# Kernel tuning notes

Measured on AMD Instinct MI355X. Metric: run time of the kernel, lower is better.

## Reference

```python
import jax, jax.numpy as jnp
import numpy as np

K = 20
EPS = 1e-5  # BatchNorm eps
SLOPE = 0.2  # LeakyReLU negative slope


def _lrelu(y):
    return jnp.where(y > 0, y, SLOPE * y)


def _knn_idx(x):
    # x: [B, C, N] -> idx [B, N, K] of nearest neighbors (largest of negative sq dist)
    inner = -2.0 * jnp.einsum('bcn,bcm->bnm', x, x)
    xx = jnp.sum(x * x, axis=1)  # [B, N]
    pd = -xx[:, :, None] - inner - xx[:, None, :]  # [B, N, N]
    return jax.lax.top_k(pd, K)[1]


def _graph_feature(x):
    # x: [B, C, N] -> [B, 2C, N, K] = cat(neighbor - center, center)
    idx = _knn_idx(x)
    xt = jnp.transpose(x, (0, 2, 1))  # [B, N, C]
    nb = jax.vmap(lambda f, i: f[i])(xt, idx)  # [B, N, K, C]
    ctr = xt[:, :, None, :]
    feat = jnp.concatenate([nb - ctr, jnp.broadcast_to(ctr, nb.shape)], axis=-1)
    return jnp.transpose(feat, (0, 3, 1, 2))


def _bn(y, p, ch_axis):
    g, b, m, v = p[0], p[1], p[2], p[3]
    shape = [1] * y.ndim
    shape[ch_axis] = -1
    scale = (g / jnp.sqrt(v + EPS)).reshape(shape)
    return (y - m.reshape(shape)) * scale + b.reshape(shape)


def _conv_block(x, w, bn):
    f = _graph_feature(x)  # [B, 2C_in, N, K]
    y = jnp.einsum('bcnk,oc->bonk', f, w)  # 1x1 conv, no bias
    y = _lrelu(_bn(y, bn, 1))
    return jnp.max(y, axis=-1)  # max over K neighbors -> [B, C_out, N]


def setup_inputs() -> dict:
    key = jax.random.key(0)
    ks = jax.random.split(key, 20)
    B, N = 8, 1024
    inp = {
        'x': jax.random.normal(ks[0], (B, 3, N), jnp.float32),
        'w0': jax.random.normal(ks[1], (64, 6), jnp.float32) * 0.1,
        'w1': jax.random.normal(ks[2], (64, 128), jnp.float32) * 0.1,
        'w2': jax.random.normal(ks[3], (128, 128), jnp.float32) * 0.1,
        'w3': jax.random.normal(ks[4], (256, 256), jnp.float32) * 0.1,
        'bn0': jax.random.uniform(ks[5], (4, 64), jnp.float32) + 0.1,
        'bn1': jax.random.uniform(ks[6], (4, 64), jnp.float32) + 0.1,
        'bn2': jax.random.uniform(ks[7], (4, 128), jnp.float32) + 0.1,
        'bn3': jax.random.uniform(ks[8], (4, 256), jnp.float32) + 0.1,
        'we': jax.random.normal(ks[9], (1024, 512), jnp.float32) * 0.05,
        'bne': jax.random.uniform(ks[10], (4, 1024), jnp.float32) + 0.1,
        'wf0': jax.random.normal(ks[11], (512, 2048), jnp.float32) * 0.02,
        'bnf0': jax.random.uniform(ks[12], (4, 512), jnp.float32) + 0.1,
        'wf1': jax.random.normal(ks[13], (256, 512), jnp.float32) * 0.05,
        'bnf1': jax.random.uniform(ks[14], (4, 256), jnp.float32) + 0.1,
        'wfin': jax.random.normal(ks[15], (64, 256), jnp.float32) * 0.05,
        'bfin': jax.random.normal(ks[16], (64,), jnp.float32) * 0.05,
    }
    return inp


def reference(x, w0, w1, w2, w3, bn0, bn1, bn2, bn3, we, bne, wf0, bnf0, wf1, bnf1, wfin, bfin):
    B = x.shape[0]
    x1 = _conv_block(x, w0, bn0)   # [B, 64, N]
    x2 = _conv_block(x1, w1, bn1)  # [B, 64, N]
    x3 = _conv_block(x2, w2, bn2)  # [B, 128, N]
    x4 = _conv_block(x3, w3, bn3)  # [B, 256, N]
    cat = jnp.concatenate([x1, x2, x3, x4], axis=1)  # [B, 512, N]
    e = _lrelu(_bn(jnp.einsum('bcn,oc->bon', cat, we), bne, 1))  # [B, 1024, N]
    p1 = jnp.max(e, axis=-1)
    p2 = jnp.mean(e, axis=-1)
    h = jnp.concatenate([p1, p2], axis=1)  # [B, 2048]
    h = _lrelu(_bn(h @ wf0.T, bnf0, 1))  # [B, 512]; dropout is eval-mode identity
    h = _lrelu(_bn(h @ wf1.T, bnf1, 1))  # [B, 256]
    return h @ wfin.T + bfin  # [B, 64]
```

## Files before the change

### kernel.cpp

```cpp
#include <hip/hip_runtime.h>
#include <math.h>

#define N_PTS 1024
#define BATCH 8
#define KNN 20
#define EPSB 1e-5f
#define SLOPE 0.2f

typedef __attribute__((ext_vector_type(8))) short short8;
typedef __attribute__((ext_vector_type(4))) float f32x4;
typedef unsigned short ushort_t;
typedef unsigned long long u64;

__device__ __forceinline__ float lrelu(float y) { return y > 0.f ? y : SLOPE * y; }

__device__ __forceinline__ ushort_t f2bf(float f) {
    union { float f; unsigned u; } v; v.f = f;
    unsigned r = v.u + 0x7FFF + ((v.u >> 16) & 1);
    return (ushort_t)(r >> 16);
}

__device__ __forceinline__ void wprep_one(const float* __restrict__ w, float* __restrict__ wpt,
                                          int C, int Cout, int g) {
    int M2 = 2 * Cout;
    if (g >= C * M2) return;
    int c = g / M2, m = g - c * M2;
    float v;
    if (m < Cout) v = w[(size_t)m * 2 * C + c];
    else { int o = m - Cout; v = w[(size_t)o * 2 * C + C + c] - w[(size_t)o * 2 * C + c]; }
    wpt[(size_t)c * M2 + m] = v;
}

__global__ void prep_kernel(const float* __restrict__ we, ushort_t* __restrict__ weh,
                            const float* __restrict__ w0, float* __restrict__ wpt0,
                            const float* __restrict__ w1, float* __restrict__ wpt1,
                            const float* __restrict__ w2, float* __restrict__ wpt2,
                            const float* __restrict__ w3, float* __restrict__ wpt3) {
    int bx = blockIdx.x, tid = threadIdx.x;
    if (bx < 512) {
        int g = bx * 256 + tid;
        float4 v = ((const float4*)we)[g];
        ushort4 o;
        o.x = f2bf(v.x); o.y = f2bf(v.y); o.z = f2bf(v.z); o.w = f2bf(v.w);
        ((ushort4*)weh)[g] = o;
    } else if (bx < 514) {
        wprep_one(w0, wpt0, 3, 64, (bx - 512) * 256 + tid);
    } else if (bx < 546) {
        wprep_one(w1, wpt1, 64, 64, (bx - 514) * 256 + tid);
    } else if (bx < 610) {
        wprep_one(w2, wpt2, 64, 128, (bx - 546) * 256 + tid);
    } else {
        wprep_one(w3, wpt3, 128, 256, (bx - 610) * 256 + tid);
    }
}

__global__ void __launch_bounds__(256)
pdabv_kernel(const float* __restrict__ x, const float* __restrict__ wpt,
             float* __restrict__ pd, float* __restrict__ A, float* __restrict__ Bv,
             int C, int Cout, int bstride) {
    int b = blockIdx.z;
    int nt = blockIdx.y;
    int bx = blockIdx.x;
    int tid = threadIdx.x;
    int tx = tid & 15, ty = tid >> 4;
    int n0 = nt * 128;
    __shared__ float sU0[16][128];
    __shared__ float sU1[16][128];
    __shared__ float sXX[256];
    const float* xb = x + (size_t)b * bstride;
    float acc[8][8] = {};
    if (bx < 8) {
        int m0 = bx * 128;
        float xxa = 0.f;
        for (int c0 = 0; c0 < C; c0 += 16) {
            for (int q = 0; q < 2; q++) {
                int f = q * 256 + tid;
                int r = f >> 5, col = (f & 31) * 4;
                int c = c0 + r;
                float4 vn = {0.f, 0.f, 0.f, 0.f}, vm = {0.f, 0.f, 0.f, 0.f};
                if (c < C) {
                    vn = *(const float4*)&xb[(size_t)c * N_PTS + n0 + col];
                    vm = *(const float4*)&xb[(size_t)c * N_PTS + m0 + col];
                }
                *(float4*)&sU0[r][col] = vn;
                *(float4*)&sU1[r][col] = vm;
            }
            __syncthreads();
            if (tid < 128) {
                for (int k = 0; k < 16; k++) { float v = sU0[k][tid]; xxa += v * v; }
            } else {
                int u = tid - 128;
                for (int k = 0; k < 16; k++) { float v = sU1[k][u]; xxa += v * v; }
            }
            for (int k = 0; k < 16; k++) {
                float4 a0 = *(const float4*)&sU0[k][ty * 4];
                float4 a1 = *(const float4*)&sU0[k][64 + ty * 4];
                float4 b0 = *(const float4*)&sU1[k][tx * 4];
                float4 b1 = *(const float4*)&sU1[k][64 + tx * 4];
                float av[8] = {a0.x, a0.y, a0.z, a0.w, a1.x, a1.y, a1.z, a1.w};
                float bw[8] = {b0.x, b0.y, b0.z, b0.w, b1.x, b1.y, b1.z, b1.w};
                for (int i = 0; i < 8; i++)
                    for (int j = 0; j < 8; j++) acc[i][j] += av[i] * bw[j];
            }
            __syncthreads();
        }
        sXX[tid] = xxa;
        __syncthreads();
        float xnv[8], xmv[8];
        for (int i = 0; i < 8; i++) xnv[i] = sXX[(i >> 2) * 64 + ty * 4 + (i & 3)];
        for (int j = 0; j < 8; j++) xmv[j] = sXX[128 + (j >> 2) * 64 + tx * 4 + (j & 3)];
        for (int i = 0; i < 8; i++) {
            int n = n0 + (i >> 2) * 64 + ty * 4 + (i & 3);
            float* prow = pd + ((size_t)(b * N_PTS + n)) * N_PTS;
            for (int jh = 0; jh < 2; jh++) {
                float4 o;
                o.x = 2.f * acc[i][jh * 4 + 0] - xnv[i] - xmv[jh * 4 + 0];
                o.y = 2.f * acc[i][jh * 4 + 1] - xnv[i] - xmv[jh * 4 + 1];
                o.z = 2.f * acc[i][jh * 4 + 2] - xnv[i] - xmv[jh * 4 + 2];
                o.w = 2.f * acc[i][jh * 4 + 3] - xnv[i] - xmv[jh * 4 + 3];
                *(float4*)&prow[m0 + jh * 64 + tx * 4] = o;
            }
        }
    } else {
        int m0 = (bx - 8) * 128;
        int M2 = 2 * Cout;
        for (int c0 = 0; c0 < C; c0 += 16) {
            for (int q = 0; q < 2; q++) {
                int f = q * 256 + tid;
                int r = f >> 5, col = (f & 31) * 4;
                int c = c0 + r;
                float4 vw = {0.f, 0.f, 0.f, 0.f}, vx = {0.f, 0.f, 0.f, 0.f};
                if (c < C) {
                    vw = *(const float4*)&wpt[(size_t)c * M2 + m0 + col];
                    vx = *(const float4*)&xb[(size_t)c * N_PTS + n0 + col];
                }
                *(float4*)&sU0[r][col] = vw;
                *(float4*)&sU1[r][col] = vx;
            }
            __syncthreads();
            for (int k = 0; k < 16; k++) {
                float4 a0 = *(const float4*)&sU0[k][ty * 4];
                float4 a1 = *(const float4*)&sU0[k][64 + ty * 4];
                float4 b0 = *(const float4*)&sU1[k][tx * 4];
                float4 b1 = *(const float4*)&sU1[k][64 + tx * 4];
                float av[8] = {a0.x, a0.y, a0.z, a0.w, a1.x, a1.y, a1.z, a1.w};
                float bw[8] = {b0.x, b0.y, b0.z, b0.w, b1.x, b1.y, b1.z, b1.w};
                for (int i = 0; i < 8; i++)
                    for (int j = 0; j < 8; j++) acc[i][j] += av[i] * bw[j];
            }
            __syncthreads();
        }
        for (int i = 0; i < 8; i++) {
            int rowm = m0 + (i >> 2) * 64 + ty * 4 + (i & 3);
            float* dst = (rowm < Cout) ? (A + ((size_t)b * Cout + rowm) * N_PTS)
                                       : (Bv + ((size_t)b * Cout + rowm - Cout) * N_PTS);
            for (int jh = 0; jh < 2; jh++) {
                float4 o;
                o.x = acc[i][jh * 4 + 0];
                o.y = acc[i][jh * 4 + 1];
                o.z = acc[i][jh * 4 + 2];
                o.w = acc[i][jh * 4 + 3];
                *(float4*)&dst[n0 + jh * 64 + tx * 4] = o;
            }
        }
    }
}

__global__ void __launch_bounds__(256)
topk_kernel(const float* __restrict__ pd, int* __restrict__ idx) {
    int wid = threadIdx.x >> 6;
    int row = blockIdx.x * 4 + wid;
    int lane = threadIdx.x & 63;
    __shared__ u64 Sk[4][64];
    const float* p = pd + (size_t)row * N_PTS;
    float v[16];
    for (int q = 0; q < 4; q++) {
        float4 t = *(const float4*)&p[lane * 16 + q * 4];
        v[q * 4 + 0] = t.x; v[q * 4 + 1] = t.y; v[q * 4 + 2] = t.z; v[q * 4 + 3] = t.w;
    }
    float lmax = v[0];
    #pragma unroll
    for (int j = 1; j < 16; j++) lmax = fmaxf(lmax, v[j]);
    float s = lmax;
    #pragma unroll
    for (int k = 2; k <= 64; k <<= 1) {
        #pragma unroll
        for (int j = k >> 1; j > 0; j >>= 1) {
            float o = __shfl_xor(s, j, 64);
            bool takeMin = (((lane & k) == 0) == ((lane & j) == 0));
            float mn = fminf(s, o), mx = fmaxf(s, o);
            s = takeMin ? mn : mx;
        }
    }
    float tp = __shfl(s, 44, 64);
    unsigned hm = 0;
    #pragma unroll
    for (int j = 0; j < 16; j++) hm |= (v[j] >= tp ? 1u : 0u) << j;
    int cnt = __popc(hm);
    int incl = cnt;
    #pragma unroll
    for (int d = 1; d < 64; d <<= 1) {
        int o = __shfl_up(incl, d, 64);
        if (lane >= d) incl += o;
    }
    int total = __shfl(incl, 63, 64);
    int pos = incl - cnt;
    if (total <= 64) {
        #pragma unroll
        for (int j = 0; j < 16; j++) {
            if (hm & (1u << j)) {
                unsigned u = __float_as_uint(v[j]);
                unsigned msk = ((unsigned)((int)u >> 31)) | 0x80000000u;
                Sk[wid][pos] = ((u64)(u ^ msk) << 32) | (unsigned)(1023 - (lane * 16 + j));
                pos++;
            }
        }
        u64 key = (lane < total) ? Sk[wid][lane] : 0ull;
        #pragma unroll
        for (int k = 2; k <= 64; k <<= 1) {
            #pragma unroll
            for (int j = k >> 1; j > 0; j >>= 1) {
                u64 o = __shfl_xor(key, j, 64);
                bool takeMin = (((lane & k) == 0) == ((lane & j) == 0));
                bool sgt = key > o;
                key = (sgt != takeMin) ? key : o;
            }
        }
        if (lane >= 44) {
            int m = 1023 - (int)(unsigned)(key & 0xFFFFFFFFu);
            idx[row * KNN + (63 - lane)] = m;
        }
    } else {
        for (int kk = 0; kk < KNN; kk++) {
            float bv = v[0]; int bj = 0;
            #pragma unroll
            for (int j = 1; j < 16; j++) if (v[j] > bv) { bv = v[j]; bj = j; }
            int bi = lane * 16 + bj;
            for (int d = 32; d > 0; d >>= 1) {
                float ov = __shfl_down(bv, d, 64);
                int oi = __shfl_down(bi, d, 64);
                if (ov > bv || (ov == bv && oi < bi)) { bv = ov; bi = oi; }
            }
            bi = __shfl(bi, 0, 64);
            if ((bi >> 4) == lane) {
                #pragma unroll
                for (int j = 0; j < 16; j++) if (j == (bi & 15)) v[j] = -INFINITY;
            }
            if (lane == 0) idx[row * KNN + kk] = bi;
        }
    }
}

__global__ void __launch_bounds__(256)
gmax_kernel(const float* __restrict__ A, const float* __restrict__ Bv,
            const int* __restrict__ idx, const float* __restrict__ bnp,
            float* __restrict__ out, int Cout, int outStrideB) {
    int b = blockIdx.z;
    int n0 = blockIdx.x * 64;
    int o0 = blockIdx.y * 4;
    int tid = threadIdx.x;
    __shared__ int sidx[64 * 21];
    __shared__ float sA[4][N_PTS];
    for (int t = tid; t < 64 * KNN; t += 256) {
        int nl = t / KNN, k = t - nl * KNN;
        sidx[nl * 21 + k] = idx[(b * N_PTS + n0) * KNN + t];
    }
    const float* Abase = A + ((size_t)b * Cout + o0) * N_PTS;
    for (int q = 0; q < 4; q++) {
        int f = q * 256 + tid;
        int r = f >> 8, c4 = (f & 255) * 4;
        *(float4*)&sA[r][c4] = *(const float4*)&Abase[(size_t)r * N_PTS + c4];
    }
    __syncthreads();
    int nl = tid & 63, ol = tid >> 6;
    float best = -INFINITY;
    #pragma unroll
    for (int k = 0; k < KNN; k++) {
        int j = sidx[nl * 21 + k];
        best = fmaxf(best, sA[ol][j]);
    }
    int o = o0 + ol;
    int n = n0 + nl;
    float pre = best + Bv[((size_t)b * Cout + o) * N_PTS + n];
    float g = bnp[o], bb = bnp[Cout + o], m = bnp[2 * Cout + o], vv = bnp[3 * Cout + o];
    float scale = g / sqrtf(vv + EPSB);
    out[(size_t)b * outStrideB + (size_t)o * N_PTS + n] = lrelu((pre - m) * scale + bb);
}

__global__ void catT_kernel(const float* __restrict__ cat, ushort_t* __restrict__ catT) {
    int b = blockIdx.z, ct = blockIdx.y, nt = blockIdx.x;
    int tid = threadIdx.x;
    __shared__ float tile[64][65];
    const float* cb = cat + (size_t)b * 512 * N_PTS;
    for (int q = 0; q < 16; q++) {
        int e = q * 256 + tid;
        int c = e >> 6, n = e & 63;
        tile[c][n] = cb[(size_t)(ct * 64 + c) * N_PTS + nt * 64 + n];
    }
    __syncthreads();
    for (int q = 0; q < 16; q++) {
        int e = q * 256 + tid;
        int n = e >> 6, c = e & 63;
        catT[((size_t)b * N_PTS + nt * 64 + n) * 512 + ct * 64 + c] = f2bf(tile[c][n]);
    }
}

__global__ void __launch_bounds__(256)
gemm6_mfma(const ushort_t* __restrict__ weh, const ushort_t* __restrict__ catT,
           const float* __restrict__ bne,
           float* __restrict__ pmax, float* __restrict__ psum) {
    int b = blockIdx.z, ot = blockIdx.y, nt = blockIdx.x;
    int tid = threadIdx.x;
    int w = tid >> 6, lane = tid & 63, q = lane >> 4, lr = lane & 15;
    int mblk = w >> 1, nblk = w & 1;
    __shared__ __align__(16) ushort_t sA[128 * 40];
    __shared__ __align__(16) ushort_t sB[128 * 40];
    __shared__ float sa[128], sc[128];
    __shared__ float redmax[128][2], redsum[128][2];
    int o0 = ot * 128, n0 = nt * 128;
    if (tid < 128) {
        int o = o0 + tid;
        float g = bne[o], bb = bne[1024 + o], m = bne[2048 + o], vv = bne[3072 + o];
        float scale = g / sqrtf(vv + EPSB);
        sa[tid] = scale; sc[tid] = bb - m * scale;
    }
    f32x4 acc[4][4] = {};
    const ushort_t* cT = catT + (size_t)b * N_PTS * 512;
    int r0 = tid >> 2, s = tid & 3;
    for (int k0 = 0; k0 < 512; k0 += 32) {
        __syncthreads();
        for (int h = 0; h < 2; h++) {
            int r = r0 + h * 64;
            *(short8*)&sA[r * 40 + s * 8] = *(const short8*)(weh + (size_t)(o0 + r) * 512 + k0 + s * 8);
            *(short8*)&sB[r * 40 + s * 8] = *(const short8*)(cT  + (size_t)(n0 + r) * 512 + k0 + s * 8);
        }
        __syncthreads();
        short8 af[4], bfr[4];
        for (int mi = 0; mi < 4; mi++)
            af[mi] = *(const short8*)&sA[(mblk * 64 + mi * 16 + lr) * 40 + q * 8];
        for (int ni = 0; ni < 4; ni++)
            bfr[ni] = *(const short8*)&sB[(nblk * 64 + ni * 16 + lr) * 40 + q * 8];
        for (int mi = 0; mi < 4; mi++)
            for (int ni = 0; ni < 4; ni++)
                acc[mi][ni] = __builtin_amdgcn_mfma_f32_16x16x32_bf16(af[mi], bfr[ni], acc[mi][ni], 0, 0, 0);
    }
    for (int mi = 0; mi < 4; mi++) {
        for (int r = 0; r < 4; r++) {
            int row = mblk * 64 + mi * 16 + q * 4 + r;
            float a = sa[row], c = sc[row];
            float mx = -INFINITY, sm = 0.f;
            for (int ni = 0; ni < 4; ni++) {
                float y = lrelu(acc[mi][ni][r] * a + c);
                mx = fmaxf(mx, y); sm += y;
            }
            for (int msk = 1; msk < 16; msk <<= 1) {
                mx = fmaxf(mx, __shfl_xor(mx, msk, 16));
                sm += __shfl_xor(sm, msk, 16);
            }
            if (lr == 0) { redmax[row][nblk] = mx; redsum[row][nblk] = sm; }
        }
    }
    __syncthreads();
    if (tid < 128) {
        float mx = fmaxf(redmax[tid][0], redmax[tid][1]);
        float sm = redsum[tid][0] + redsum[tid][1];
        int o = o0 + tid;
        pmax[((size_t)(b * 1024 + o)) * 8 + nt] = mx;
        psum[((size_t)(b * 1024 + o)) * 8 + nt] = sm;
    }
}

__global__ void pool_reduce_kernel(const float* __restrict__ pmax, const float* __restrict__ psum,
                                   float* __restrict__ h0) {
    int g = blockIdx.x * 256 + threadIdx.x;
    int b = g >> 10, o = g & 1023;
    float mx = -INFINITY, sm = 0.f;
    for (int t = 0; t < 8; t++) { mx = fmaxf(mx, pmax[g * 8 + t]); sm += psum[g * 8 + t]; }
    h0[(size_t)b * 2048 + o] = mx;
    h0[(size_t)b * 2048 + 1024 + o] = sm * (1.0f / 1024.0f);
}

__global__ void fc_kernel(const float* __restrict__ in, const float* __restrict__ w,
                          const float* __restrict__ bnp, const float* __restrict__ bias,
                          float* __restrict__ out, int Cin, int Cout, int mode) {
    int blk = blockIdx.x;
    int b = blk / Cout, o = blk % Cout;
    int lane = threadIdx.x;
    const float* inb = in + (size_t)b * Cin;
    const float* wo = w + (size_t)o * Cin;
    float acc = 0.f;
    for (int c = lane; c < Cin; c += 64) acc += inb[c] * wo[c];
    for (int s = 32; s > 0; s >>= 1) acc += __shfl_down(acc, s, 64);
    if (lane == 0) {
        float y = acc;
        if (mode == 0) {
            float g = bnp[o], bb = bnp[Cout + o], m = bnp[2 * Cout + o], vv = bnp[3 * Cout + o];
            y = lrelu((y - m) * (g / sqrtf(vv + EPSB)) + bb);
        } else {
            y += bias[o];
        }
        out[(size_t)b * Cout + o] = y;
    }
}

extern "C" void kernel_launch(void* const* d_in, const int* in_sizes, int n_in,
                              void* d_out, int out_size, void* d_ws, size_t ws_size,
                              hipStream_t stream) {
    const float* x    = (const float*)d_in[0];
    const float* w0   = (const float*)d_in[1];
    const float* w1   = (const float*)d_in[2];
    const float* w2   = (const float*)d_in[3];
    const float* w3   = (const float*)d_in[4];
    const float* bn0  = (const float*)d_in[5];
    const float* bn1  = (const float*)d_in[6];
    const float* bn2  = (const float*)d_in[7];
    const float* bn3  = (const float*)d_in[8];
    const float* we   = (const float*)d_in[9];
    const float* bne  = (const float*)d_in[10];
    const float* wf0  = (const float*)d_in[11];
    const float* bnf0 = (const float*)d_in[12];
    const float* wf1  = (const float*)d_in[13];
    const float* bnf1 = (const float*)d_in[14];
    const float* wfin = (const float*)d_in[15];
    const float* bfin = (const float*)d_in[16];

    float* ws = (float*)d_ws;
    size_t off = 0;
    float* cat  = ws + off; off += (size_t)BATCH * 512 * N_PTS;
    float* pd   = ws + off; off += (size_t)BATCH * N_PTS * N_PTS;
    float* A    = ws + off; off += (size_t)BATCH * 256 * N_PTS;
    float* Bv   = ws + off; off += (size_t)BATCH * 256 * N_PTS;
    float* pmax = ws + off; off += (size_t)BATCH * N_PTS * 8;
    float* psum = ws + off; off += (size_t)BATCH * N_PTS * 8;
    float* h0   = ws + off; off += (size_t)BATCH * 2048;
    float* h1   = ws + off; off += (size_t)BATCH * 512;
    float* h2   = ws + off; off += (size_t)BATCH * 256;
    int*   idx  = (int*)(ws + off); off += (size_t)BATCH * N_PTS * KNN;
    ushort_t* weh  = (ushort_t*)(ws + off); off += (size_t)(1024 * 512) / 2;
    ushort_t* catT = (ushort_t*)(ws + off); off += (size_t)BATCH * N_PTS * 512 / 2;
    float* wpt0 = ws + off; off += 3 * 128;
    float* wpt1 = ws + off; off += 64 * 128;
    float* wpt2 = ws + off; off += 64 * 256;
    float* wpt3 = ws + off; off += 128 * 512;

    const int CSTR = 512 * N_PTS;
    const int topkBlocks = BATCH * N_PTS / 4;

    prep_kernel<<<866, 256, 0, stream>>>(we, weh, w0, wpt0, w1, wpt1, w2, wpt2, w3, wpt3);

    pdabv_kernel<<<dim3(9, 8, BATCH), 256, 0, stream>>>(x, wpt0, pd, A, Bv, 3, 64, 3 * N_PTS);
    topk_kernel<<<topkBlocks, 256, 0, stream>>>(pd, idx);
    gmax_kernel<<<dim3(16, 16, BATCH), 256, 0, stream>>>(A, Bv, idx, bn0, cat, 64, CSTR);

    pdabv_kernel<<<dim3(9, 8, BATCH), 256, 0, stream>>>(cat, wpt1, pd, A, Bv, 64, 64, CSTR);
    topk_kernel<<<topkBlocks, 256, 0, stream>>>(pd, idx);
    gmax_kernel<<<dim3(16, 16, BATCH), 256, 0, stream>>>(A, Bv, idx, bn1, cat + 64 * N_PTS, 64, CSTR);

    pdabv_kernel<<<dim3(10, 8, BATCH), 256, 0, stream>>>(cat + 64 * N_PTS, wpt2, pd, A, Bv, 64, 128, CSTR);
    topk_kernel<<<topkBlocks, 256, 0, stream>>>(pd, idx);
    gmax_kernel<<<dim3(16, 32, BATCH), 256, 0, stream>>>(A, Bv, idx, bn2, cat + 128 * N_PTS, 128, CSTR);

    pdabv_kernel<<<dim3(12, 8, BATCH), 256, 0, stream>>>(cat + 128 * N_PTS, wpt3, pd, A, Bv, 128, 256, CSTR);
    topk_kernel<<<topkBlocks, 256, 0, stream>>>(pd, idx);
    gmax_kernel<<<dim3(16, 64, BATCH), 256, 0, stream>>>(A, Bv, idx, bn3, cat + 256 * N_PTS, 256, CSTR);

    catT_kernel<<<dim3(16, 8, BATCH), 256, 0, stream>>>(cat, catT);
    gemm6_mfma<<<dim3(8, 8, BATCH), 256, 0, stream>>>(weh, catT, bne, pmax, psum);
    pool_reduce_kernel<<<32, 256, 0, stream>>>(pmax, psum, h0);

    fc_kernel<<<BATCH * 512, 64, 0, stream>>>(h0, wf0, bnf0, nullptr, h1, 2048, 512, 0);
    fc_kernel<<<BATCH * 256, 64, 0, stream>>>(h1, wf1, bnf1, nullptr, h2, 512, 256, 0);
    fc_kernel<<<BATCH * 64, 64, 0, stream>>>(h2, wfin, nullptr, bfin, (float*)d_out, 256, 64, 1);
}
```

Measured before the change: 331.6 us.

## Fuse pairwise-distance computation with top-k selection, eliminating the pd buffer

Merges the pairwise-distance GEMM and the top-k kernel into one kernel. Each block computes a 16-row by 1024-column strip of distances in registers and runs the bitonic-threshold top-k selection on it directly. This removes the 32 MB write and re-read of the distance matrix per layer, plus one launch per layer. The A/Bv projection path is retiled to 64x64, and the kernel uses a 64 KB swizzled shared buffer holding the whole point set for each channel chunk. The trade-off is fewer, heavier blocks (64 per batch for distances) and recomputation of the full row of points per block, which lowers parallelism.

After: 425.3 us. 1.28x slower.

```diff
diff --git a/kernel.cpp b/kernel.cpp
--- a/kernel.cpp
+++ b/kernel.cpp
@@ -19,6 +19,8 @@
     unsigned r = v.u + 0x7FFF + ((v.u >> 16) & 1);
     return (ushort_t)(r >> 16);
 }
+
+__device__ __forceinline__ int fswz(int i) { return i ^ (((i >> 5) & 7) << 2); }
 
 __device__ __forceinline__ void wprep_one(const float* __restrict__ w, float* __restrict__ wpt,
                                           int C, int Cout, int g) {
@@ -54,199 +56,201 @@
     }
 }
 
-__global__ void __launch_bounds__(256)
-pdabv_kernel(const float* __restrict__ x, const float* __restrict__ wpt,
-             float* __restrict__ pd, float* __restrict__ A, float* __restrict__ Bv,
-             int C, int Cout, int bstride) {
-    int b = blockIdx.z;
-    int nt = blockIdx.y;
+__global__ void __launch_bounds__(256, 2)
+pdknn_abv_kernel(const float* __restrict__ x, const float* __restrict__ wpt,
+                 int* __restrict__ idx, float* __restrict__ A, float* __restrict__ Bv,
+                 int C, int Cout, int bstride) {
+    __shared__ float sB[16 * 1024];
+    __shared__ float sXX[1024];
+    __shared__ u64 Sk[4][64];
+    int tid = threadIdx.x;
+    int b = blockIdx.y;
     int bx = blockIdx.x;
-    int tid = threadIdx.x;
-    int tx = tid & 15, ty = tid >> 4;
-    int n0 = nt * 128;
-    __shared__ float sU0[16][128];
-    __shared__ float sU1[16][128];
-    __shared__ float sXX[256];
     const float* xb = x + (size_t)b * bstride;
-    float acc[8][8] = {};
-    if (bx < 8) {
-        int m0 = bx * 128;
-        float xxa = 0.f;
+
+    if (bx < 64) {
+        int n0 = bx * 16;
+        int lane = tid & 63, w = tid >> 6;
+        float acc[4][16];
+        #pragma unroll
+        for (int i = 0; i < 4; i++)
+            #pragma unroll
+            for (int j = 0; j < 16; j++) acc[i][j] = 0.f;
+        float xxv[4] = {0.f, 0.f, 0.f, 0.f};
+        int colw = tid * 4;
+        int gsw = fswz(colw);
+        int offA = fswz(n0 + w * 4);
+        int offB0 = fswz(lane * 16);
+        int offB1 = fswz(lane * 16 + 4);
+        int offB2 = fswz(lane * 16 + 8);
+        int offB3 = fswz(lane * 16 + 12);
+
         for (int c0 = 0; c0 < C; c0 += 16) {
-            for (int q = 0; q < 2; q++) {
-                int f = q * 256 + tid;
-                int r = f >> 5, col = (f & 31) * 4;
-                int c = c0 + r;
-                float4 vn = {0.f, 0.f, 0.f, 0.f}, vm = {0.f, 0.f, 0.f, 0.f};
-                if (c < C) {
-                    vn = *(const float4*)&xb[(size_t)c * N_PTS + n0 + col];
-                    vm = *(const float4*)&xb[(size_t)c * N_PTS + m0 + col];
+            __syncthreads();
+            #pragma unroll
+            for (int q = 0; q < 16; q++) {
+                float4 vx = {0.f, 0.f, 0.f, 0.f};
+                int c = c0 + q;
+                if (c < C) vx = *(const float4*)&xb[(size_t)c * N_PTS + colw];
+                xxv[0] += vx.x * vx.x; xxv[1] += vx.y * vx.y;
+                xxv[2] += vx.z * vx.z; xxv[3] += vx.w * vx.w;
+                *(float4*)&sB[q * 1024 + gsw] = vx;
+            }
+            __syncthreads();
+            #pragma unroll
+            for (int k = 0; k < 16; k++) {
+                const float* rowp = &sB[k * 1024];
+                float4 a4 = *(const float4*)&rowp[offA];
+                float4 b0 = *(const float4*)&rowp[offB0];
+                float4 b1 = *(const float4*)&rowp[offB1];
+                float4 b2 = *(const float4*)&rowp[offB2];
+                float4 b3 = *(const float4*)&rowp[offB3];
+                float av[4] = {a4.x, a4.y, a4.z, a4.w};
+                float bw[16] = {b0.x, b0.y, b0.z, b0.w, b1.x, b1.y, b1.z, b1.w,
+                                b2.x, b2.y, b2.z, b2.w, b3.x, b3.y, b3.z, b3.w};
+                #pragma unroll
+                for (int i = 0; i < 4; i++)
+                    #pragma unroll
+                    for (int j = 0; j < 16; j++) acc[i][j] += av[i] * bw[j];
+            }
+        }
+        *(float4*)&sXX[gsw] = *(float4*)&xxv[0];
+        __syncthreads();
+        float xxm[16];
+        {
+            float4 t0 = *(const float4*)&sXX[offB0];
+            float4 t1 = *(const float4*)&sXX[offB1];
+            float4 t2 = *(const float4*)&sXX[offB2];
+            float4 t3 = *(const float4*)&sXX[offB3];
+            xxm[0] = t0.x; xxm[1] = t0.y; xxm[2] = t0.z; xxm[3] = t0.w;
+            xxm[4] = t1.x; xxm[5] = t1.y; xxm[6] = t1.z; xxm[7] = t1.w;
+            xxm[8] = t2.x; xxm[9] = t2.y; xxm[10] = t2.z; xxm[11] = t2.w;
+            xxm[12] = t3.x; xxm[13] = t3.y; xxm[14] = t3.z; xxm[15] = t3.w;
+        }
+        #pragma unroll
+        for (int ri = 0; ri < 4; ri++) {
+            int n = n0 + w * 4 + ri;
+            float xxn = sXX[fswz(n)];
+            float v[16];
+            #pragma unroll
+            for (int j = 0; j < 16; j++) v[j] = 2.f * acc[ri][j] - xxn - xxm[j];
+            float lmax = v[0];
+            #pragma unroll
+            for (int j = 1; j < 16; j++) lmax = fmaxf(lmax, v[j]);
+            float s = lmax;
+            #pragma unroll
+            for (int kk = 2; kk <= 64; kk <<= 1) {
+                #pragma unroll
+                for (int j = kk >> 1; j > 0; j >>= 1) {
+                    float o = __shfl_xor(s, j, 64);
+                    bool takeMin = (((lane & kk) == 0) == ((lane & j) == 0));
+                    float mn = fminf(s, o), mx = fmaxf(s, o);
+                    s = takeMin ? mn : mx;
                 }
-                *(float4*)&sU0[r][col] = vn;
-                *(float4*)&sU1[r][col] = vm;
-            }
+            }
+            float tp = __shfl(s, 44, 64);
+            unsigned hm = 0;
+            #pragma unroll
+            for (int j = 0; j < 16; j++) hm |= (v[j] >= tp ? 1u : 0u) << j;
+            int cnt = __popc(hm);
+            int incl = cnt;
+            #pragma unroll
+            for (int d = 1; d < 64; d <<= 1) {
+                int o = __shfl_up(incl, d, 64);
+                if (lane >= d) incl += o;
+            }
+            int total = __shfl(incl, 63, 64);
+            int pos = incl - cnt;
+            int row = b * N_PTS + n;
+            if (total <= 64) {
+                #pragma unroll
+                for (int j = 0; j < 16; j++) {
+                    if (hm & (1u << j)) {
+                        unsigned u = __float_as_uint(v[j]);
+                        unsigned msk2 = ((unsigned)((int)u >> 31)) | 0x80000000u;
+                        Sk[w][pos] = ((u64)(u ^ msk2) << 32) | (unsigned)(1023 - (lane * 16 + j));
+                        pos++;
+                    }
+                }
+                u64 key = (lane < total) ? Sk[w][lane] : 0ull;
+                #pragma unroll
+                for (int kk = 2; kk <= 64; kk <<= 1) {
+                    #pragma unroll
+                    for (int j = kk >> 1; j > 0; j >>= 1) {
+                        u64 o = __shfl_xor(key, j, 64);
+                        bool takeMin = (((lane & kk) == 0) == ((lane & j) == 0));
+                        bool sgt = key > o;
+                        key = (sgt != takeMin) ? key : o;
+                    }
+                }
+                if (lane >= 44) {
+                    int m = 1023 - (int)(unsigned)(key & 0xFFFFFFFFu);
+                    idx[row * KNN + (63 - lane)] = m;
+                }
+            } else {
+                for (int kk = 0; kk < KNN; kk++) {
+                    float bv2 = v[0]; int bj = 0;
+                    #pragma unroll
+                    for (int j = 1; j < 16; j++) if (v[j] > bv2) { bv2 = v[j]; bj = j; }
+                    int bi = lane * 16 + bj;
+                    for (int d = 32; d > 0; d >>= 1) {
+                        float ov = __shfl_down(bv2, d, 64);
+                        int oi = __shfl_down(bi, d, 64);
+                        if (ov > bv2 || (ov == bv2 && oi < bi)) { bv2 = ov; bi = oi; }
+                    }
+                    bi = __shfl(bi, 0, 64);
+                    if ((bi >> 4) == lane) {
+                        #pragma unroll
+                        for (int j = 0; j < 16; j++) if (j == (bi & 15)) v[j] = -INFINITY;
+                    }
+                    if (lane == 0) idx[row * KNN + kk] = bi;
+                }
+            }
+        }
+    } else {
+        int bx2 = bx - 64;
+        int mt = bx2 >> 4, nt = bx2 & 15;
+        int m0 = mt * 64, n0 = nt * 64;
+        int M2 = 2 * Cout;
+        float* sW = sB;
+        float* sX = sB + 1024;
+        int tx = tid & 15, ty = tid >> 4;
+        float acc[4][4];
+        #pragma unroll
+        for (int i = 0; i < 4; i++)
+            #pragma unroll
+            for (int j = 0; j < 4; j++) acc[i][j] = 0.f;
+        int r = tid >> 4, col4 = (tid & 15) * 4;
+        for (int c0 = 0; c0 < C; c0 += 16) {
             __syncthreads();
-            if (tid < 128) {
-                for (int k = 0; k < 16; k++) { float v = sU0[k][tid]; xxa += v * v; }
-            } else {
-                int u = tid - 128;
-                for (int k = 0; k < 16; k++) { float v = sU1[k][u]; xxa += v * v; }
-            }
+            float4 vw = {0.f, 0.f, 0.f, 0.f}, vx = {0.f, 0.f, 0.f, 0.f};
+            int c = c0 + r;
+            if (c < C) {
+                vw = *(const float4*)&wpt[(size_t)c * M2 + m0 + col4];
+                vx = *(const float4*)&xb[(size_t)c * N_PTS + n0 + col4];
+            }
+            *(float4*)&sW[r * 64 + col4] = vw;
+            *(float4*)&sX[r * 64 + col4] = vx;
+            __syncthreads();
+            #pragma unroll
             for (int k = 0; k < 16; k++) {
-                float4 a0 = *(const float4*)&sU0[k][ty * 4];
-                float4 a1 = *(const float4*)&sU0[k][64 + ty * 4];
-                float4 b0 = *(const float4*)&sU1[k][tx * 4];
-                float4 b1 = *(const float4*)&sU1[k][64 + tx * 4];
-                float av[8] = {a0.x, a0.y, a0.z, a0.w, a1.x, a1.y, a1.z, a1.w};
-                float bw[8] = {b0.x, b0.y, b0.z, b0.w, b1.x, b1.y, b1.z, b1.w};
-                for (int i = 0; i < 8; i++)
-                    for (int j = 0; j < 8; j++) acc[i][j] += av[i] * bw[j];
-            }
-            __syncthreads();
-        }
-        sXX[tid] = xxa;
-        __syncthreads();
-        float xnv[8], xmv[8];
-        for (int i = 0; i < 8; i++) xnv[i] = sXX[(i >> 2) * 64 + ty * 4 + (i & 3)];
-        for (int j = 0; j < 8; j++) xmv[j] = sXX[128 + (j >> 2) * 64 + tx * 4 + (j & 3)];
-        for (int i = 0; i < 8; i++) {
-            int n = n0 + (i >> 2) * 64 + ty * 4 + (i & 3);
-            float* prow = pd + ((size_t)(b * N_PTS + n)) * N_PTS;
-            for (int jh = 0; jh < 2; jh++) {
-                float4 o;
-                o.x = 2.f * acc[i][jh * 4 + 0] - xnv[i] - xmv[jh * 4 + 0];
-                o.y = 2.f * acc[i][jh * 4 + 1] - xnv[i] - xmv[jh * 4 + 1];
-                o.z = 2.f * acc[i][jh * 4 + 2] - xnv[i] - xmv[jh * 4 + 2];
-                o.w = 2.f * acc[i][jh * 4 + 3] - xnv[i] - xmv[jh * 4 + 3];
-                *(float4*)&prow[m0 + jh * 64 + tx * 4] = o;
-            }
-        }
-    } else {
-        int m0 = (bx - 8) * 128;
-        int M2 = 2 * Cout;
-        for (int c0 = 0; c0 < C; c0 += 16) {
-            for (int q = 0; q < 2; q++) {
-                int f = q * 256 + tid;
-                int r = f >> 5, col = (f & 31) * 4;
-                int c = c0 + r;
-                float4 vw = {0.f, 0.f, 0.f, 0.f}, vx = {0.f, 0.f, 0.f, 0.f};
-                if (c < C) {
-                    vw = *(const float4*)&wpt[(size_t)c * M2 + m0 + col];
-                    vx = *(const float4*)&xb[(size_t)c * N_PTS + n0 + col];
-                }
-                *(float4*)&sU0[r][col] = vw;
-                *(float4*)&sU1[r][col] = vx;
-            }
-            __syncthreads();
-            for (int k = 0; k < 16; k++) {
-                float4 a0 = *(const float4*)&sU0[k][ty * 4];
-                float4 a1 = *(const float4*)&sU0[k][64 + ty * 4];
-                float4 b0 = *(const float4*)&sU1[k][tx * 4];
-                float4 b1 = *(const float4*)&sU1[k][64 + tx * 4];
-                float av[8] = {a0.x, a0.y, a0.z, a0.w, a1.x, a1.y, a1.z, a1.w};
-                float bw[8] = {b0.x, b0.y, b0.z, b0.w, b1.x, b1.y, b1.z, b1.w};
-                for (int i = 0; i < 8; i++)
-                    for (int j = 0; j < 8; j++) acc[i][j] += av[i] * bw[j];
-            }
-            __syncthreads();
-        }
-        for (int i = 0; i < 8; i++) {
-            int rowm = m0 + (i >> 2) * 64 + ty * 4 + (i & 3);
+                float4 a4 = *(const float4*)&sW[k * 64 + ty * 4];
+                float4 b4 = *(const float4*)&sX[k * 64 + tx * 4];
+                float av[4] = {a4.x, a4.y, a4.z, a4.w};
+                float bw[4] = {b4.x, b4.y, b4.z, b4.w};
+                #pragma unroll
+                for (int i = 0; i < 4; i++)
+                    #pragma unroll
+                    for (int j = 0; j < 4; j++) acc[i][j] += av[i] * bw[j];
+            }
+        }
+        #pragma unroll
+        for (int i = 0; i < 4; i++) {
+            int rowm = m0 + ty * 4 + i;
             float* dst = (rowm < Cout) ? (A + ((size_t)b * Cout + rowm) * N_PTS)
                                        : (Bv + ((size_t)b * Cout + rowm - Cout) * N_PTS);
-            for (int jh = 0; jh < 2; jh++) {
-                float4 o;
-                o.x = acc[i][jh * 4 + 0];
-                o.y = acc[i][jh * 4 + 1];
-                o.z = acc[i][jh * 4 + 2];
-                o.w = acc[i][jh * 4 + 3];
-                *(float4*)&dst[n0 + jh * 64 + tx * 4] = o;
-            }
-        }
-    }
-}
-
-__global__ void __launch_bounds__(256)
-topk_kernel(const float* __restrict__ pd, int* __restrict__ idx) {
-    int wid = threadIdx.x >> 6;
-    int row = blockIdx.x * 4 + wid;
-    int lane = threadIdx.x & 63;
-    __shared__ u64 Sk[4][64];
-    const float* p = pd + (size_t)row * N_PTS;
-    float v[16];
-    for (int q = 0; q < 4; q++) {
-        float4 t = *(const float4*)&p[lane * 16 + q * 4];
-        v[q * 4 + 0] = t.x; v[q * 4 + 1] = t.y; v[q * 4 + 2] = t.z; v[q * 4 + 3] = t.w;
-    }
-    float lmax = v[0];
-    #pragma unroll
-    for (int j = 1; j < 16; j++) lmax = fmaxf(lmax, v[j]);
-    float s = lmax;
-    #pragma unroll
-    for (int k = 2; k <= 64; k <<= 1) {
-        #pragma unroll
-        for (int j = k >> 1; j > 0; j >>= 1) {
-            float o = __shfl_xor(s, j, 64);
-            bool takeMin = (((lane & k) == 0) == ((lane & j) == 0));
-            float mn = fminf(s, o), mx = fmaxf(s, o);
-            s = takeMin ? mn : mx;
-        }
-    }
-    float tp = __shfl(s, 44, 64);
-    unsigned hm = 0;
-    #pragma unroll
-    for (int j = 0; j < 16; j++) hm |= (v[j] >= tp ? 1u : 0u) << j;
-    int cnt = __popc(hm);
-    int incl = cnt;
-    #pragma unroll
-    for (int d = 1; d < 64; d <<= 1) {
-        int o = __shfl_up(incl, d, 64);
-        if (lane >= d) incl += o;
-    }
-    int total = __shfl(incl, 63, 64);
-    int pos = incl - cnt;
-    if (total <= 64) {
-        #pragma unroll
-        for (int j = 0; j < 16; j++) {
-            if (hm & (1u << j)) {
-                unsigned u = __float_as_uint(v[j]);
-                unsigned msk = ((unsigned)((int)u >> 31)) | 0x80000000u;
-                Sk[wid][pos] = ((u64)(u ^ msk) << 32) | (unsigned)(1023 - (lane * 16 + j));
-                pos++;
-            }
-        }
-        u64 key = (lane < total) ? Sk[wid][lane] : 0ull;
-        #pragma unroll
-        for (int k = 2; k <= 64; k <<= 1) {
-            #pragma unroll
-            for (int j = k >> 1; j > 0; j >>= 1) {
-                u64 o = __shfl_xor(key, j, 64);
-                bool takeMin = (((lane & k) == 0) == ((lane & j) == 0));
-                bool sgt = key > o;
-                key = (sgt != takeMin) ? key : o;
-            }
-        }
-        if (lane >= 44) {
-            int m = 1023 - (int)(unsigned)(key & 0xFFFFFFFFu);
-            idx[row * KNN + (63 - lane)] = m;
-        }
-    } else {
-        for (int kk = 0; kk < KNN; kk++) {
-            float bv = v[0]; int bj = 0;
-            #pragma unroll
-            for (int j = 1; j < 16; j++) if (v[j] > bv) { bv = v[j]; bj = j; }
-            int bi = lane * 16 + bj;
-            for (int d = 32; d > 0; d >>= 1) {
-                float ov = __shfl_down(bv, d, 64);
-                int oi = __shfl_down(bi, d, 64);
-                if (ov > bv || (ov == bv && oi < bi)) { bv = ov; bi = oi; }
-            }
-            bi = __shfl(bi, 0, 64);
-            if ((bi >> 4) == lane) {
-                #pragma unroll
-                for (int j = 0; j < 16; j++) if (j == (bi & 15)) v[j] = -INFINITY;
-            }
-            if (lane == 0) idx[row * KNN + kk] = bi;
+            float4 o = {acc[i][0], acc[i][1], acc[i][2], acc[i][3]};
+            *(float4*)&dst[n0 + tx * 4] = o;
         }
     }
 }
@@ -427,7 +431,6 @@
     float* ws = (float*)d_ws;
     size_t off = 0;
     float* cat  = ws + off; off += (size_t)BATCH * 512 * N_PTS;
-    float* pd   = ws + off; off += (size_t)BATCH * N_PTS * N_PTS;
     float* A    = ws + off; off += (size_t)BATCH * 256 * N_PTS;
     float* Bv   = ws + off; off += (size_t)BATCH * 256 * N_PTS;
     float* pmax = ws + off; off += (size_t)BATCH * N_PTS * 8;
@@ -444,24 +447,19 @@
     float* wpt3 = ws + off; off += 128 * 512;
 
     const int CSTR = 512 * N_PTS;
-    const int topkBlocks = BATCH * N_PTS / 4;
 
     prep_kernel<<<866, 256, 0, stream>>>(we, weh, w0, wpt0, w1, wpt1, w2, wpt2, w3, wpt3);
 
-    pdabv_kernel<<<dim3(9, 8, BATCH), 256, 0, stream>>>(x, wpt0, pd, A, Bv, 3, 64, 3 * N_PTS);
-    topk_kernel<<<topkBlocks, 256, 0, stream>>>(pd, idx);
+    pdknn_abv_kernel<<<dim3(64 + 32, BATCH), 256, 0, stream>>>(x, wpt0, idx, A, Bv, 3, 64, 3 * N_PTS);
     gmax_kernel<<<dim3(16, 16, BATCH), 256, 0, stream>>>(A, Bv, idx, bn0, cat, 64, CSTR);
 
-    pdabv_kernel<<<dim3(9, 8, BATCH), 256, 0, stream>>>(cat, wpt1, pd, A, Bv, 64, 64, CSTR);
-    topk_kernel<<<topkBlocks, 256, 0, stream>>>(pd, idx);
+    pdknn_abv_kernel<<<dim3(64 + 32, BATCH), 256, 0, stream>>>(cat, wpt1, idx, A, Bv, 64, 64, CSTR);
     gmax_kernel<<<dim3(16, 16, BATCH), 256, 0, stream>>>(A, Bv, idx, bn1, cat + 64 * N_PTS, 64, CSTR);
 
-    pdabv_kernel<<<dim3(10, 8, BATCH), 256, 0, stream>>>(cat + 64 * N_PTS, wpt2, pd, A, Bv, 64, 128, CSTR);
-    topk_kernel<<<topkBlocks, 256, 0, stream>>>(pd, idx);
+    pdknn_abv_kernel<<<dim3(64 + 64, BATCH), 256, 0, stream>>>(cat + 64 * N_PTS, wpt2, idx, A, Bv, 64, 128, CSTR);
     gmax_kernel<<<dim3(16, 32, BATCH), 256, 0, stream>>>(A, Bv, idx, bn2, cat + 128 * N_PTS, 128, CSTR);
 
-    pdabv_kernel<<<dim3(12, 8, BATCH), 256, 0, stream>>>(cat + 128 * N_PTS, wpt3, pd, A, Bv, 128, 256, CSTR);
-    topk_kernel<<<topkBlocks, 256, 0, stream>>>(pd, idx);
+    pdknn_abv_kernel<<<dim3(64 + 128, BATCH), 256, 0, stream>>>(cat + 128 * N_PTS, wpt3, idx, A, Bv, 128, 256, CSTR);
     gmax_kernel<<<dim3(16, 64, BATCH), 256, 0, stream>>>(A, Bv, idx, bn3, cat + 256 * N_PTS, 256, CSTR);
 
     catT_kernel<<<dim3(16, 8, BATCH), 256, 0, stream>>>(cat, catT);
```

## Double-buffer pdabv tiles and precompute squared norms in a separate kernel

Applied to the files above, without the earlier changes.

The pairwise-distance/projection kernel now uses two shared-memory buffers. The next channel tile is prefetched into registers while the current tile is being multiplied, which removes one barrier per iteration and hides global-load latency. Squared norms are computed by a small new xx_kernel, and the distance output drops the row-constant -xx[n] term, which does not change per-row top-k selection. The loops are fully unrolled. The cost is doubled shared memory, more registers, and four extra kernel launches.

Result: slower. 476.9 us (+43.8%).

```diff
diff --git a/kernel.cpp b/kernel.cpp
--- a/kernel.cpp
+++ b/kernel.cpp
@@ -54,8 +54,20 @@
     }
 }
 
+__global__ void __launch_bounds__(64)
+xx_kernel(const float* __restrict__ x, float* __restrict__ xx, int C, int bstride) {
+    int b = blockIdx.y;
+    int n = blockIdx.x * 64 + threadIdx.x;
+    const float* xb = x + (size_t)b * bstride + n;
+    float s = 0.f;
+    #pragma unroll 4
+    for (int c = 0; c < C; c++) { float v = xb[(size_t)c * N_PTS]; s += v * v; }
+    xx[b * N_PTS + n] = s;
+}
+
 __global__ void __launch_bounds__(256)
 pdabv_kernel(const float* __restrict__ x, const float* __restrict__ wpt,
+             const float* __restrict__ xx,
              float* __restrict__ pd, float* __restrict__ A, float* __restrict__ Bv,
              int C, int Cout, int bstride) {
     int b = blockIdx.z;
@@ -64,92 +76,103 @@
     int tid = threadIdx.x;
     int tx = tid & 15, ty = tid >> 4;
     int n0 = nt * 128;
-    __shared__ float sU0[16][128];
-    __shared__ float sU1[16][128];
-    __shared__ float sXX[256];
+    __shared__ float sU0[2][16][128];
+    __shared__ float sU1[2][16][128];
     const float* xb = x + (size_t)b * bstride;
+
+    const float* p0; const float* p1; int s0, s1, m0;
+    if (bx < 8) { m0 = bx * 128;       p0 = xb + n0;  p1 = xb + m0; s0 = N_PTS;    s1 = N_PTS; }
+    else        { m0 = (bx - 8) * 128; p0 = wpt + m0; p1 = xb + n0; s0 = 2 * Cout; s1 = N_PTS; }
+
     float acc[8][8] = {};
-    if (bx < 8) {
-        int m0 = bx * 128;
-        float xxa = 0.f;
-        for (int c0 = 0; c0 < C; c0 += 16) {
-            for (int q = 0; q < 2; q++) {
-                int f = q * 256 + tid;
-                int r = f >> 5, col = (f & 31) * 4;
-                int c = c0 + r;
-                float4 vn = {0.f, 0.f, 0.f, 0.f}, vm = {0.f, 0.f, 0.f, 0.f};
-                if (c < C) {
-                    vn = *(const float4*)&xb[(size_t)c * N_PTS + n0 + col];
-                    vm = *(const float4*)&xb[(size_t)c * N_PTS + m0 + col];
-                }
-                *(float4*)&sU0[r][col] = vn;
-                *(float4*)&sU1[r][col] = vm;
-            }
-            __syncthreads();
-            if (tid < 128) {
-                for (int k = 0; k < 16; k++) { float v = sU0[k][tid]; xxa += v * v; }
-            } else {
-                int u = tid - 128;
-                for (int k = 0; k < 16; k++) { float v = sU1[k][u]; xxa += v * v; }
-            }
+    float4 r0[2], r1[2];
+    int fr0 = tid >> 5, fr1 = (256 + tid) >> 5;
+    int fc = (tid & 31) * 4;
+
+    {
+        float4 z = {0.f, 0.f, 0.f, 0.f};
+        r0[0] = (fr0 < C) ? *(const float4*)&p0[(size_t)fr0 * s0 + fc] : z;
+        r1[0] = (fr0 < C) ? *(const float4*)&p1[(size_t)fr0 * s1 + fc] : z;
+        r0[1] = (fr1 < C) ? *(const float4*)&p0[(size_t)fr1 * s0 + fc] : z;
+        r1[1] = (fr1 < C) ? *(const float4*)&p1[(size_t)fr1 * s1 + fc] : z;
+        *(float4*)&sU0[0][fr0][fc] = r0[0];
+        *(float4*)&sU1[0][fr0][fc] = r1[0];
+        *(float4*)&sU0[0][fr1][fc] = r0[1];
+        *(float4*)&sU1[0][fr1][fc] = r1[1];
+    }
+    __syncthreads();
+
+    int nc = (C + 15) >> 4;
+    for (int cc = 0; cc < nc; cc++) {
+        int cur = cc & 1;
+        if (cc + 1 < nc) {
+            int c0 = (cc + 1) * 16;
+            float4 z = {0.f, 0.f, 0.f, 0.f};
+            int ca = c0 + fr0, cb = c0 + fr1;
+            r0[0] = (ca < C) ? *(const float4*)&p0[(size_t)ca * s0 + fc] : z;
+            r1[0] = (ca < C) ? *(const float4*)&p1[(size_t)ca * s1 + fc] : z;
+            r0[1] = (cb < C) ? *(const float4*)&p0[(size_t)cb * s0 + fc] : z;
+            r1[1] = (cb < C) ? *(const float4*)&p1[(size_t)cb * s1 + fc] : z;
+        }
+        int kmax = C - cc * 16; if (kmax > 16) kmax = 16;
+        if (kmax == 16) {
+            #pragma unroll
             for (int k = 0; k < 16; k++) {
-                float4 a0 = *(const float4*)&sU0[k][ty * 4];
-                float4 a1 = *(const float4*)&sU0[k][64 + ty * 4];
-                float4 b0 = *(const float4*)&sU1[k][tx * 4];
-                float4 b1 = *(const float4*)&sU1[k][64 + tx * 4];
+                float4 a0 = *(const float4*)&sU0[cur][k][ty * 4];
+                float4 a1 = *(const float4*)&sU0[cur][k][64 + ty * 4];
+                float4 b0 = *(const float4*)&sU1[cur][k][tx * 4];
+                float4 b1 = *(const float4*)&sU1[cur][k][64 + tx * 4];
                 float av[8] = {a0.x, a0.y, a0.z, a0.w, a1.x, a1.y, a1.z, a1.w};
                 float bw[8] = {b0.x, b0.y, b0.z, b0.w, b1.x, b1.y, b1.z, b1.w};
+                #pragma unroll
                 for (int i = 0; i < 8; i++)
+                    #pragma unroll
                     for (int j = 0; j < 8; j++) acc[i][j] += av[i] * bw[j];
             }
-            __syncthreads();
-        }
-        sXX[tid] = xxa;
+        } else {
+            for (int k = 0; k < kmax; k++) {
+                float4 a0 = *(const float4*)&sU0[cur][k][ty * 4];
+                float4 a1 = *(const float4*)&sU0[cur][k][64 + ty * 4];
+                float4 b0 = *(const float4*)&sU1[cur][k][tx * 4];
+                float4 b1 = *(const float4*)&sU1[cur][k][64 + tx * 4];
+                float av[8] = {a0.x, a0.y, a0.z, a0.w, a1.x, a1.y, a1.z, a1.w};
+                float bw[8] = {b0.x, b0.y, b0.z, b0.w, b1.x, b1.y, b1.z, b1.w};
+                #pragma unroll
+                for (int i = 0; i < 8; i++)
+                    #pragma unroll
+                    for (int j = 0; j < 8; j++) acc[i][j] += av[i] * bw[j];
+            }
+        }
+        if (cc + 1 < nc) {
+            int nb = cur ^ 1;
+            *(float4*)&sU0[nb][fr0][fc] = r0[0];
+            *(float4*)&sU1[nb][fr0][fc] = r1[0];
+            *(float4*)&sU0[nb][fr1][fc] = r0[1];
+            *(float4*)&sU1[nb][fr1][fc] = r1[1];
+        }
         __syncthreads();
-        float xnv[8], xmv[8];
-        for (int i = 0; i < 8; i++) xnv[i] = sXX[(i >> 2) * 64 + ty * 4 + (i & 3)];
-        for (int j = 0; j < 8; j++) xmv[j] = sXX[128 + (j >> 2) * 64 + tx * 4 + (j & 3)];
+    }
+
+    if (bx < 8) {
+        float xm[8];
+        const float* xxb = xx + b * N_PTS + m0;
+        *(float4*)&xm[0] = *(const float4*)&xxb[tx * 4];
+        *(float4*)&xm[4] = *(const float4*)&xxb[64 + tx * 4];
+        #pragma unroll
         for (int i = 0; i < 8; i++) {
             int n = n0 + (i >> 2) * 64 + ty * 4 + (i & 3);
-            float* prow = pd + ((size_t)(b * N_PTS + n)) * N_PTS;
+            float* prow = pd + ((size_t)(b * N_PTS + n)) * N_PTS + m0;
             for (int jh = 0; jh < 2; jh++) {
                 float4 o;
-                o.x = 2.f * acc[i][jh * 4 + 0] - xnv[i] - xmv[jh * 4 + 0];
-                o.y = 2.f * acc[i][jh * 4 + 1] - xnv[i] - xmv[jh * 4 + 1];
-                o.z = 2.f * acc[i][jh * 4 + 2] - xnv[i] - xmv[jh * 4 + 2];
-                o.w = 2.f * acc[i][jh * 4 + 3] - xnv[i] - xmv[jh * 4 + 3];
-                *(float4*)&prow[m0 + jh * 64 + tx * 4] = o;
+                o.x = 2.f * acc[i][jh * 4 + 0] - xm[jh * 4 + 0];
+                o.y = 2.f * acc[i][jh * 4 + 1] - xm[jh * 4 + 1];
+                o.z = 2.f * acc[i][jh * 4 + 2] - xm[jh * 4 + 2];
+                o.w = 2.f * acc[i][jh * 4 + 3] - xm[jh * 4 + 3];
+                *(float4*)&prow[jh * 64 + tx * 4] = o;
             }
         }
     } else {
-        int m0 = (bx - 8) * 128;
-        int M2 = 2 * Cout;
-        for (int c0 = 0; c0 < C; c0 += 16) {
-            for (int q = 0; q < 2; q++) {
-                int f = q * 256 + tid;
-                int r = f >> 5, col = (f & 31) * 4;
-                int c = c0 + r;
-                float4 vw = {0.f, 0.f, 0.f, 0.f}, vx = {0.f, 0.f, 0.f, 0.f};
-                if (c < C) {
-                    vw = *(const float4*)&wpt[(size_t)c * M2 + m0 + col];
-                    vx = *(const float4*)&xb[(size_t)c * N_PTS + n0 + col];
-                }
-                *(float4*)&sU0[r][col] = vw;
-                *(float4*)&sU1[r][col] = vx;
-            }
-            __syncthreads();
-            for (int k = 0; k < 16; k++) {
-                float4 a0 = *(const float4*)&sU0[k][ty * 4];
-                float4 a1 = *(const float4*)&sU0[k][64 + ty * 4];
-                float4 b0 = *(const float4*)&sU1[k][tx * 4];
-                float4 b1 = *(const float4*)&sU1[k][64 + tx * 4];
-                float av[8] = {a0.x, a0.y, a0.z, a0.w, a1.x, a1.y, a1.z, a1.w};
-                float bw[8] = {b0.x, b0.y, b0.z, b0.w, b1.x, b1.y, b1.z, b1.w};
-                for (int i = 0; i < 8; i++)
-                    for (int j = 0; j < 8; j++) acc[i][j] += av[i] * bw[j];
-            }
-            __syncthreads();
-        }
+        #pragma unroll
         for (int i = 0; i < 8; i++) {
             int rowm = m0 + (i >> 2) * 64 + ty * 4 + (i & 3);
             float* dst = (rowm < Cout) ? (A + ((size_t)b * Cout + rowm) * N_PTS)
@@ -430,6 +453,7 @@
     float* pd   = ws + off; off += (size_t)BATCH * N_PTS * N_PTS;
     float* A    = ws + off; off += (size_t)BATCH * 256 * N_PTS;
     float* Bv   = ws + off; off += (size_t)BATCH * 256 * N_PTS;
+    float* xxv  = ws + off; off += (size_t)BATCH * N_PTS;
     float* pmax = ws + off; off += (size_t)BATCH * N_PTS * 8;
     float* psum = ws + off; off += (size_t)BATCH * N_PTS * 8;
     float* h0   = ws + off; off += (size_t)BATCH * 2048;
@@ -448,19 +472,23 @@
 
     prep_kernel<<<866, 256, 0, stream>>>(we, weh, w0, wpt0, w1, wpt1, w2, wpt2, w3, wpt3);
 
-    pdabv_kernel<<<dim3(9, 8, BATCH), 256, 0, stream>>>(x, wpt0, pd, A, Bv, 3, 64, 3 * N_PTS);
+    xx_kernel<<<dim3(16, BATCH), 64, 0, stream>>>(x, xxv, 3, 3 * N_PTS);
+    pdabv_kernel<<<dim3(9, 8, BATCH), 256, 0, stream>>>(x, wpt0, xxv, pd, A, Bv, 3, 64, 3 * N_PTS);
     topk_kernel<<<topkBlocks, 256, 0, stream>>>(pd, idx);
     gmax_kernel<<<dim3(16, 16, BATCH), 256, 0, stream>>>(A, Bv, idx, bn0, cat, 64, CSTR);
 
-    pdabv_kernel<<<dim3(9, 8, BATCH), 256, 0, stream>>>(cat, wpt1, pd, A, Bv, 64, 64, CSTR);
+    xx_kernel<<<dim3(16, BATCH), 64, 0, stream>>>(cat, xxv, 64, CSTR);
+    pdabv_kernel<<<dim3(9, 8, BATCH), 256, 0, stream>>>(cat, wpt1, xxv, pd, A, Bv, 64, 64, CSTR);
     topk_kernel<<<topkBlocks, 256, 0, stream>>>(pd, idx);
     gmax_kernel<<<dim3(16, 16, BATCH), 256, 0, stream>>>(A, Bv, idx, bn1, cat + 64 * N_PTS, 64, CSTR);
 
-    pdabv_kernel<<<dim3(10, 8, BATCH), 256, 0, stream>>>(cat + 64 * N_PTS, wpt2, pd, A, Bv, 64, 128, CSTR);
+    xx_kernel<<<dim3(16, BATCH), 64, 0, stream>>>(cat + 64 * N_PTS, xxv, 64, CSTR);
+    pdabv_kernel<<<dim3(10, 8, BATCH), 256, 0, stream>>>(cat + 64 * N_PTS, wpt2, xxv, pd, A, Bv, 64, 128, CSTR);
     topk_kernel<<<topkBlocks, 256, 0, stream>>>(pd, idx);
     gmax_kernel<<<dim3(16, 32, BATCH), 256, 0, stream>>>(A, Bv, idx, bn2, cat + 128 * N_PTS, 128, CSTR);
 
-    pdabv_kernel<<<dim3(12, 8, BATCH), 256, 0, stream>>>(cat + 128 * N_PTS, wpt3, pd, A, Bv, 128, 256, CSTR);
+    xx_kernel<<<dim3(16, BATCH), 64, 0, stream>>>(cat + 128 * N_PTS, xxv, 128, CSTR);
+    pdabv_kernel<<<dim3(12, 8, BATCH), 256, 0, stream>>>(cat + 128 * N_PTS, wpt3, xxv, pd, A, Bv, 128, 256, CSTR);
     topk_kernel<<<topkBlocks, 256, 0, stream>>>(pd, idx);
     gmax_kernel<<<dim3(16, 64, BATCH), 256, 0, stream>>>(A, Bv, idx, bn3, cat + 256 * N_PTS, 256, CSTR);
 
```
